# Performance work log

Hardware: AMD Instinct MI355X
Metric: run time of the kernel (lower is better)

## Reference

```python
import jax, jax.numpy as jnp
import numpy as np

B, T, N_EMBD, HEAD = 8, 2048, 1024, 64
NEG_INF = -1e30  # stand-in for float('-inf'), safe under fp16/bf16 after where


def setup_inputs() -> dict:
    key = jax.random.key(0)
    k0, k1, k2, k3 = jax.random.split(key, 4)
    idx = jax.random.normal(k0, (B, T, N_EMBD), dtype=jnp.float32)
    # nn.Linear weights have shape (out_features, in_features)
    Wk = jax.random.normal(k1, (HEAD, N_EMBD), dtype=jnp.float32) * 0.02
    Wq = jax.random.normal(k2, (HEAD, N_EMBD), dtype=jnp.float32) * 0.02
    Wv = jax.random.normal(k3, (HEAD, N_EMBD), dtype=jnp.float32) * 0.02
    return {"idx": idx, "Wk": Wk, "Wq": Wq, "Wv": Wv}


def reference(idx, Wk, Wq, Wv):
    # idx: [B,T,C]; W*: [H,C] (torch Linear layout, y = x @ W.T)
    Tn = idx.shape[1]
    k = jnp.einsum('btc,hc->bth', idx, Wk)
    q = jnp.einsum('btc,hc->bth', idx, Wq)
    v = jnp.einsum('btc,hc->bth', idx, Wv)
    # NOTE: original has NO 1/sqrt(head_size) scaling
    wei = jnp.einsum('bth,bsh->bts', q, k)  # [B,T,T]
    causal = jnp.tril(jnp.ones((Tn, Tn), dtype=bool))  # keep where tril != 0
    wei = jnp.where(causal[None, :, :], wei, NEG_INF)
    # NOTE: original softmaxes over dim=1 (query axis), not the last axis
    wei = jax.nn.softmax(wei, axis=1)
    out = jnp.einsum('bts,bsh->bth', wei, v)  # [B,T,H]
    return out
```

## Files before the change

kernel.cpp:

```cpp
#include <hip/hip_runtime.h>


typedef __attribute__((ext_vector_type(8))) short bf16x8;
typedef __attribute__((ext_vector_type(4))) float f32x4;
typedef unsigned short u16;

#define MFMA(a, b, c) __builtin_amdgcn_mfma_f32_16x16x32_bf16((a), (b), (c), 0, 0, 0)

__device__ __forceinline__ u16 f2bf(float x) {
    unsigned u = __float_as_uint(x);
    u += 0x7fff + ((u >> 16) & 1);
    return (u16)(u >> 16);
}
__device__ __forceinline__ float bf2f(u16 h) {
    return __uint_as_float(((unsigned)h) << 16);
}

__device__ __forceinline__ void split8(const f32x4 x0, const f32x4 x1,
                                       bf16x8* hv, bf16x8* lv)
{
    const float f[8] = {x0[0], x0[1], x0[2], x0[3], x1[0], x1[1], x1[2], x1[3]};
    union { unsigned u[4]; bf16x8 v; } H, L;
    #pragma unroll
    for (int j = 0; j < 4; ++j) {
        const unsigned u0 = __float_as_uint(f[2 * j]);
        const unsigned u1 = __float_as_uint(f[2 * j + 1]);
        H.u[j] = __builtin_amdgcn_perm(u1, u0, 0x07060302);
        const float l0 = f[2 * j]     - __uint_as_float(u0 & 0xffff0000u);
        const float l1 = f[2 * j + 1] - __uint_as_float(u1 & 0xffff0000u);
        L.u[j] = __builtin_amdgcn_perm(__float_as_uint(l1), __float_as_uint(l0),
                                       0x07060302);
    }
    *hv = H.v;
    *lv = L.v;
}

typedef const __attribute__((address_space(1))) void* gas_p;
typedef __attribute__((address_space(3))) void* las_p;

#define WH_OFF  0u
#define WL_OFF  (WH_OFF + 192u*1024u*2u)
#define FQH_OFF (WL_OFF + 192u*1024u*2u)
#define FQL_OFF (FQH_OFF + 2u*1024u*1024u)
#define FKH_OFF (FQL_OFF + 2u*1024u*1024u)
#define FKL_OFF (FKH_OFF + 2u*1024u*1024u)
#define VF_OFF  (FKL_OFF + 2u*1024u*1024u)
#define DD_OFF  (VF_OFF + 2u*1024u*1024u)
#define PF_OFF  (DD_OFF + 8u*2048u*4u)

__global__ __launch_bounds__(128) void wsplit_kernel(
    const float* __restrict__ Wk, const float* __restrict__ Wq,
    const float* __restrict__ Wv, u16* __restrict__ FWH)
{
    const int n = blockIdx.x;
    const int nblk = n >> 4, lr = n & 15;
    const float* src = (n < 64) ? (Wq + (long)n * 1024)
                     : (n < 128) ? (Wk + (long)(n - 64) * 1024)
                                 : (Wv + (long)(n - 128) * 1024);
    const int f = threadIdx.x;
    const int kc = f >> 2, q = f & 3;
    const float4 f0 = *(const float4*)&src[kc * 32 + q * 8];
    const float4 f1 = *(const float4*)&src[kc * 32 + q * 8 + 4];
    const float vs[8] = {f0.x, f0.y, f0.z, f0.w, f1.x, f1.y, f1.z, f1.w};
    bf16x8 hv;
    #pragma unroll
    for (int j = 0; j < 8; ++j) hv[j] = (short)f2bf(vs[j]);
    const long o = ((long)(nblk * 32 + kc) * 64 + q * 16 + lr) * 8;
    *(bf16x8*)&FWH[o] = hv;
}

__global__ __launch_bounds__(512, 2) void qkv_kernel(
    const float* __restrict__ idx, const u16* __restrict__ FWH,
    u16* __restrict__ FQH, u16* __restrict__ FQL,
    u16* __restrict__ FKH, u16* __restrict__ FKL, u16* __restrict__ VF)
{
    __shared__ __align__(16) char smem[3][40960];
    const int tid = threadIdx.x;
    const int w = tid >> 6, lr = tid & 15, quad = (tid >> 4) & 3;
    const int lane = tid & 63;
    const int r0 = blockIdx.x * 64;
    const int b = r0 >> 11, t0 = r0 & 2047;
    const int m0 = (w & 1) * 32;
    const int nbb = (w >> 1) * 3;

    const float* asrc[2];
    int adst[2];
    #pragma unroll
    for (int j = 0; j < 2; ++j) {
        const int s = w * 2 + j;
        const int row = s * 4 + (lane >> 4);
        const int lc = (lane & 15) ^ (row & 7);
        asrc[j] = idx + (long)(r0 + row) * 1024 + lc * 4;
        adst[j] = s * 1024;
    }
    const u16* fsrc[3];
    int fdst[3];
    #pragma unroll
    for (int j = 0; j < 3; ++j) {
        const int seg = w * 3 + j;
        const int nblk = seg >> 1, kcl = seg & 1;
        fsrc[j] = FWH + (long)nblk * 16384 + kcl * 512 + lane * 8;
        fdst[j] = 16384 + seg * 1024;
    }

#define ISSUE(PH)                                                             \
    {                                                                         \
        const int nb_ = (PH) % 3;                                             \
        _Pragma("unroll")                                                     \
        for (int j = 0; j < 2; ++j)                                           \
            __builtin_amdgcn_global_load_lds((gas_p)(asrc[j] + (PH) * 64),    \
                (las_p)(smem[nb_] + adst[j]), 16, 0, 0);                      \
        _Pragma("unroll")                                                     \
        for (int j = 0; j < 3; ++j)                                           \
            __builtin_amdgcn_global_load_lds((gas_p)(fsrc[j] + (long)(PH) * 1024), \
                (las_p)(smem[nb_] + fdst[j]), 16, 0, 0);                      \
    }

#define COMPUTE(PH)                                                           \
    {                                                                         \
        const int nb_ = (PH) % 3;                                             \
        const float* A_ = (const float*)smem[nb_];                            \
        const u16* F_ = (const u16*)(smem[nb_] + 16384);                      \
        _Pragma("unroll")                                                     \
        for (int kc = 0; kc < 2; ++kc) {                                      \
            bf16x8 AH[2], AL[2];                                              \
            _Pragma("unroll")                                                 \
            for (int mi = 0; mi < 2; ++mi) {                                  \
                const int R = m0 + mi * 16 + lr;                              \
                const int c0 = (kc * 8 + quad * 2) ^ (lr & 7);                \
                const f32x4 x0 = *(const f32x4*)&A_[R * 64 + c0 * 4];         \
                const f32x4 x1 = *(const f32x4*)&A_[R * 64 + (c0 ^ 1) * 4];   \
                split8(x0, x1, &AH[mi], &AL[mi]);                             \
            }                                                                 \
            _Pragma("unroll")                                                 \
            for (int nf = 0; nf < 3; ++nf) {                                  \
                const int sb = (((nbb + nf) * 2 + kc)) * 512 + lane * 8;      \
                const bf16x8 bh = *(const bf16x8*)&F_[sb];                    \
                _Pragma("unroll")                                             \
                for (int mi = 0; mi < 2; ++mi) {                              \
                    f32x4 c = acc[mi][nf];                                    \
                    c = MFMA(AH[mi], bh, c);                                  \
                    c = MFMA(AL[mi], bh, c);                                  \
                    acc[mi][nf] = c;                                          \
                }                                                             \
            }                                                                 \
        }                                                                     \
    }

#define WAITV(N)                                                              \
    asm volatile("s_waitcnt vmcnt(" #N ")" ::: "memory");                     \
    __builtin_amdgcn_sched_barrier(0);                                        \
    __builtin_amdgcn_s_barrier();

    f32x4 acc[2][3] = {};

    ISSUE(0); ISSUE(1);
    WAITV(5)

    for (int ph = 0; ph < 14; ++ph) {
        ISSUE(ph + 2);
        __builtin_amdgcn_sched_barrier(0);
        COMPUTE(ph);
        WAITV(5)
    }
    COMPUTE(14);
    WAITV(0)
    COMPUTE(15);

#undef WAITV
#undef COMPUTE
#undef ISSUE

    #pragma unroll
    for (int mi = 0; mi < 2; ++mi) {
        const int tb = t0 + m0 + mi * 16 + quad * 4;
        const int tblk = (t0 + m0 + mi * 16) >> 4;
        #pragma unroll
        for (int nf = 0; nf < 3; ++nf) {
            const int n = (nbb + nf) * 16 + lr;
            const f32x4 a = acc[mi][nf];
            if (n < 128) {
                u16* Hd = (n < 64) ? FQH : FKH;
                u16* Ld = (n < 64) ? FQL : FKL;
                const int h = n & 63;
                const int kc = h >> 5;
                const int lsub = 16 * ((h & 31) >> 3);
                const long base = ((long)(b * 128 + tblk) * 2 + kc) * 512 + (h & 7);
                #pragma unroll
                for (int r = 0; r < 4; ++r) {
                    const float v = a[r];
                    const u16 hi = f2bf(v);
                    const u16 lo = f2bf(v - bf2f(hi));
                    const long o = base + (long)(quad * 4 + r + lsub) * 8;
                    Hd[o] = hi; Ld[o] = lo;
                }
            } else {
                const int h = n - 128;
                const int hblk = h >> 4;
                #pragma unroll
                for (int r = 0; r < 4; ++r) {
                    const int t = tb + r;
                    const long o = ((long)(b * 4 + hblk) * 64 + (t >> 5)) * 512
                                 + (long)(16 * ((t & 31) >> 3) + (h & 15)) * 8 + (t & 7);
                    VF[o] = f2bf(a[r]);
                }
            }
        }
    }
}

__global__ __launch_bounds__(256, 4) void stats_kernel(
    const u16* __restrict__ FQH, const u16* __restrict__ FQL,
    const u16* __restrict__ FKH, const u16* __restrict__ FKL,
    u16* __restrict__ PF, float* __restrict__ D)
{
    __shared__ float red[4][64];
    __shared__ __align__(16) u16 p_l[64 * 64];
    const int tid = threadIdx.x;
    const int w = tid >> 6, lr = tid & 15, quad = (tid >> 4) & 3;
    const int lane = tid & 63;
    const int b = blockIdx.y;
    int x = blockIdx.x, i = 0;
    for (;;) { const int nc = (35 - i) >> 2; if (x < nc) break; x -= nc; ++i; }
    const int s0 = i * 64;
    const int jt0 = i + 4 * x, jt1 = min(jt0 + 4, 32);

    bf16x8 KH[4][2], KL[4][2];
    #pragma unroll
    for (int sf = 0; sf < 4; ++sf) {
        const long kb = ((long)(b * 128 + i * 4 + sf) * 2) * 512 + lane * 8;
        KH[sf][0] = *(const bf16x8*)&FKH[kb];
        KH[sf][1] = *(const bf16x8*)&FKH[kb + 512];
        KL[sf][0] = *(const bf16x8*)&FKL[kb];
        KL[sf][1] = *(const bf16x8*)&FKL[kb + 512];
    }

    float dsum[4][4] = {};
    for (int jt = jt0; jt < jt1; ++jt) {
        const long qb = ((long)(b * 128 + jt * 4 + w) * 2) * 512 + lane * 8;
        const bf16x8 qh0 = *(const bf16x8*)&FQH[qb];
        const bf16x8 qh1 = *(const bf16x8*)&FQH[qb + 512];
        const bf16x8 ql0 = *(const bf16x8*)&FQL[qb];
        const bf16x8 ql1 = *(const bf16x8*)&FQL[qb + 512];
        const bool diag = (jt == i);
        const int t_sub = w * 16 + lr;
        #pragma unroll
        for (int sf = 0; sf < 4; ++sf) {
            f32x4 cc = {};
            cc = MFMA(KH[sf][0], qh0, cc);
            cc = MFMA(KH[sf][0], ql0, cc);
            cc = MFMA(KL[sf][0], qh0, cc);
            cc = MFMA(KH[sf][1], qh1, cc);
            cc = MFMA(KH[sf][1], ql1, cc);
            cc = MFMA(KL[sf][1], qh1, cc);

            u16 hq[4];
            #pragma unroll
            for (int r = 0; r < 4; ++r) {
                float ev = __expf(cc[r]);
                if (diag && (t_sub < sf * 16 + quad * 4 + r)) ev = 0.f;
                dsum[sf][r] += ev;
                hq[r] = f2bf(ev);
            }
            const int s_sub = sf * 16 + quad * 4;
            const int ch = (s_sub >> 3) ^ (t_sub & 7);
            const int aoff = t_sub * 64 + ch * 8 + (s_sub & 7);
            uint2 pk;
            pk.x = (unsigned)hq[0] | ((unsigned)hq[1] << 16);
            pk.y = (unsigned)hq[2] | ((unsigned)hq[3] << 16);
            *(uint2*)&p_l[aoff] = pk;
        }
        __syncthreads();
        #pragma unroll
        for (int kcp = 0; kcp < 2; ++kcp) {
            const int row = w * 16 + (lane & 15);
            const int sc = kcp * 32 + (lane >> 4) * 8;
            const int ch = (sc >> 3) ^ (row & 7);
            const bf16x8 v = *(const bf16x8*)&p_l[row * 64 + ch * 8];
            const long o = ((long)(b * 128 + jt * 4 + w) * 64 + i * 2 + kcp) * 512
                         + lane * 8;
            *(bf16x8*)&PF[o] = v;
        }
        __syncthreads();
    }

    #pragma unroll
    for (int sf = 0; sf < 4; ++sf)
        #pragma unroll
        for (int r = 0; r < 4; ++r) {
            float v = dsum[sf][r];
            v += __shfl_xor(v, 1);
            v += __shfl_xor(v, 2);
            v += __shfl_xor(v, 4);
            v += __shfl_xor(v, 8);
            dsum[sf][r] = v;
        }
    if (lr == 0) {
        #pragma unroll
        for (int sf = 0; sf < 4; ++sf)
            #pragma unroll
            for (int r = 0; r < 4; ++r)
                red[w][sf * 16 + quad * 4 + r] = dsum[sf][r];
    }
    __syncthreads();
    if (tid < 64)
        atomicAdd(&D[b * 2048 + s0 + tid],
                  red[0][tid] + red[1][tid] + red[2][tid] + red[3][tid]);
}

__global__ __launch_bounds__(256) void vscale_kernel(
    u16* __restrict__ VF, const float* __restrict__ D)
{
    const int g = blockIdx.x * 256 + threadIdx.x;
    const long e = (long)g * 8;
    const int lane = (int)((e >> 3) & 63);
    const int kc   = (int)((e >> 9) & 63);
    const int b    = (int)(e >> 17);
    const int s = kc * 32 + (lane >> 4) * 8;
    const float4 d0 = *(const float4*)&D[b * 2048 + s];
    const float4 d1 = *(const float4*)&D[b * 2048 + s + 4];
    const float dv[8] = {d0.x, d0.y, d0.z, d0.w, d1.x, d1.y, d1.z, d1.w};
    bf16x8 vv = *(bf16x8*)&VF[e];
    bf16x8 ov;
    #pragma unroll
    for (int j = 0; j < 8; ++j)
        ov[j] = (short)f2bf(bf2f((u16)vv[j]) / dv[j]);
    *(bf16x8*)&VF[e] = ov;
}

__global__ __launch_bounds__(256, 4) void out_kernel(
    const u16* __restrict__ PF, const u16* __restrict__ VF,
    float* __restrict__ out)
{
    const int tid = threadIdx.x;
    const int w = tid >> 6, lr = tid & 15, quad = (tid >> 4) & 3;
    const int lane = tid & 63;
    const int b = blockIdx.y;
    int x = blockIdx.x, i = 0;
    for (;;) { const int nc = (i + 8) >> 3; if (x < nc) break; x -= nc; ++i; }
    const int t0 = i * 64;
    const int js0 = 8 * x, js1 = min(8 * x + 8, i + 1);
    const int tblk = i * 4 + w;

    f32x4 oacc[4] = {};
    for (int js = js0; js < js1; ++js) {
        const long pb = ((long)(b * 128 + tblk) * 64 + 2 * js) * 512 + lane * 8;
        const bf16x8 a0 = *(const bf16x8*)&PF[pb];
        const bf16x8 a1 = *(const bf16x8*)&PF[pb + 512];
        #pragma unroll
        for (int nf = 0; nf < 4; ++nf) {
            const long vb = ((long)(b * 4 + nf) * 64 + 2 * js) * 512 + lane * 8;
            const bf16x8 v0 = *(const bf16x8*)&VF[vb];
            const bf16x8 v1 = *(const bf16x8*)&VF[vb + 512];
            oacc[nf] = MFMA(a0, v0, oacc[nf]);
            oacc[nf] = MFMA(a1, v1, oacc[nf]);
        }
    }

    const bool single = (i < 8);
    #pragma unroll
    for (int nf = 0; nf < 4; ++nf) {
        const int h = nf * 16 + lr;
        #pragma unroll
        for (int r = 0; r < 4; ++r) {
            const int t = t0 + w * 16 + quad * 4 + r;
            const long o = (long)(b * 2048 + t) * 64 + h;
            if (single) out[o] = oacc[nf][r];
            else        atomicAdd(&out[o], oacc[nf][r]);
        }
    }
}

extern "C" void kernel_launch(void* const* d_in, const int* in_sizes, int n_in,
                              void* d_out, int out_size, void* d_ws, size_t ws_size,
                              hipStream_t stream)
{
    const float* idx = (const float*)d_in[0];
    const float* Wk  = (const float*)d_in[1];
    const float* Wq  = (const float*)d_in[2];
    const float* Wv  = (const float*)d_in[3];
    char* ws = (char*)d_ws;
    float* out = (float*)d_out;

    u16* FWH = (u16*)(ws + WH_OFF);
    u16* FQH = (u16*)(ws + FQH_OFF); u16* FQL = (u16*)(ws + FQL_OFF);
    u16* FKH = (u16*)(ws + FKH_OFF); u16* FKL = (u16*)(ws + FKL_OFF);
    u16* VF  = (u16*)(ws + VF_OFF);
    float* Dp = (float*)(ws + DD_OFF);
    u16* PF  = (u16*)(ws + PF_OFF);

    hipMemsetAsync(out, 0, (size_t)8 * 2048 * 64 * sizeof(float), stream);
    hipMemsetAsync(Dp, 0, (size_t)8 * 2048 * sizeof(float), stream);

    wsplit_kernel<<<192, 128, 0, stream>>>(Wk, Wq, Wv, FWH);
    qkv_kernel<<<256, 512, 0, stream>>>(idx, FWH, FQH, FQL, FKH, FKL, VF);
    stats_kernel<<<dim3(144, 8), 256, 0, stream>>>(FQH, FQL, FKH, FKL, PF, Dp);
    vscale_kernel<<<512, 256, 0, stream>>>(VF, Dp);
    out_kernel<<<dim3(80, 8), 256, 0, stream>>>(PF, VF, out);
}
```

Baseline: 149.8 us.

## Recompute exp(QK) in output kernel instead of storing P matrix

The stats kernel now only accumulates the column softmax denominators and no longer writes the bf16 probability matrix to global memory. The output kernel recomputes the QK^T scores (split-bf16, six MFMAs per tile), exponentiates, masks and stages them through LDS before multiplying with the scaled V. This removes a large global write and read of the T×T probability tiles. In exchange it duplicates the score MFMAs and exp work and adds block barriers and LDS to out_kernel, with its occupancy hint lowered to 2.

```diff
diff --git a/kernel.cpp b/kernel.cpp
--- a/kernel.cpp
+++ b/kernel.cpp
@@ -39,14 +39,12 @@
 typedef __attribute__((address_space(3))) void* las_p;
 
 #define WH_OFF  0u
-#define WL_OFF  (WH_OFF + 192u*1024u*2u)
-#define FQH_OFF (WL_OFF + 192u*1024u*2u)
+#define FQH_OFF (WH_OFF + 2u*192u*1024u*2u)
 #define FQL_OFF (FQH_OFF + 2u*1024u*1024u)
 #define FKH_OFF (FQL_OFF + 2u*1024u*1024u)
 #define FKL_OFF (FKH_OFF + 2u*1024u*1024u)
 #define VF_OFF  (FKL_OFF + 2u*1024u*1024u)
 #define DD_OFF  (VF_OFF + 2u*1024u*1024u)
-#define PF_OFF  (DD_OFF + 8u*2048u*4u)
 
 __global__ __launch_bounds__(128) void wsplit_kernel(
     const float* __restrict__ Wk, const float* __restrict__ Wq,
@@ -212,10 +210,9 @@
 __global__ __launch_bounds__(256, 4) void stats_kernel(
     const u16* __restrict__ FQH, const u16* __restrict__ FQL,
     const u16* __restrict__ FKH, const u16* __restrict__ FKL,
-    u16* __restrict__ PF, float* __restrict__ D)
+    float* __restrict__ D)
 {
     __shared__ float red[4][64];
-    __shared__ __align__(16) u16 p_l[64 * 64];
     const int tid = threadIdx.x;
     const int w = tid >> 6, lr = tid & 15, quad = (tid >> 4) & 3;
     const int lane = tid & 63;
@@ -253,35 +250,13 @@
             cc = MFMA(KH[sf][1], qh1, cc);
             cc = MFMA(KH[sf][1], ql1, cc);
             cc = MFMA(KL[sf][1], qh1, cc);
-
-            u16 hq[4];
             #pragma unroll
             for (int r = 0; r < 4; ++r) {
                 float ev = __expf(cc[r]);
                 if (diag && (t_sub < sf * 16 + quad * 4 + r)) ev = 0.f;
                 dsum[sf][r] += ev;
-                hq[r] = f2bf(ev);
             }
-            const int s_sub = sf * 16 + quad * 4;
-            const int ch = (s_sub >> 3) ^ (t_sub & 7);
-            const int aoff = t_sub * 64 + ch * 8 + (s_sub & 7);
-            uint2 pk;
-            pk.x = (unsigned)hq[0] | ((unsigned)hq[1] << 16);
-            pk.y = (unsigned)hq[2] | ((unsigned)hq[3] << 16);
-            *(uint2*)&p_l[aoff] = pk;
-        }
-        __syncthreads();
-        #pragma unroll
-        for (int kcp = 0; kcp < 2; ++kcp) {
-            const int row = w * 16 + (lane & 15);
-            const int sc = kcp * 32 + (lane >> 4) * 8;
-            const int ch = (sc >> 3) ^ (row & 7);
-            const bf16x8 v = *(const bf16x8*)&p_l[row * 64 + ch * 8];
-            const long o = ((long)(b * 128 + jt * 4 + w) * 64 + i * 2 + kcp) * 512
-                         + lane * 8;
-            *(bf16x8*)&PF[o] = v;
-        }
-        __syncthreads();
+        }
     }
 
     #pragma unroll
@@ -328,10 +303,12 @@
     *(bf16x8*)&VF[e] = ov;
 }
 
-__global__ __launch_bounds__(256, 4) void out_kernel(
-    const u16* __restrict__ PF, const u16* __restrict__ VF,
-    float* __restrict__ out)
-{
+__global__ __launch_bounds__(256, 2) void out_kernel(
+    const u16* __restrict__ FQH, const u16* __restrict__ FQL,
+    const u16* __restrict__ FKH, const u16* __restrict__ FKL,
+    const u16* __restrict__ VF, float* __restrict__ out)
+{
+    __shared__ __align__(16) u16 p_l[64 * 64];
     const int tid = threadIdx.x;
     const int w = tid >> 6, lr = tid & 15, quad = (tid >> 4) & 3;
     const int lane = tid & 63;
@@ -340,21 +317,66 @@
     for (;;) { const int nc = (i + 8) >> 3; if (x < nc) break; x -= nc; ++i; }
     const int t0 = i * 64;
     const int js0 = 8 * x, js1 = min(8 * x + 8, i + 1);
-    const int tblk = i * 4 + w;
+
+    const long qb = ((long)(b * 128 + i * 4 + w) * 2) * 512 + lane * 8;
+    const bf16x8 qh0 = *(const bf16x8*)&FQH[qb];
+    const bf16x8 qh1 = *(const bf16x8*)&FQH[qb + 512];
+    const bf16x8 ql0 = *(const bf16x8*)&FQL[qb];
+    const bf16x8 ql1 = *(const bf16x8*)&FQL[qb + 512];
+    const int t_sub = w * 16 + lr;
 
     f32x4 oacc[4] = {};
     for (int js = js0; js < js1; ++js) {
-        const long pb = ((long)(b * 128 + tblk) * 64 + 2 * js) * 512 + lane * 8;
-        const bf16x8 a0 = *(const bf16x8*)&PF[pb];
-        const bf16x8 a1 = *(const bf16x8*)&PF[pb + 512];
+        const bool diag = (js == i);
+        #pragma unroll
+        for (int sf = 0; sf < 4; ++sf) {
+            const long kb = ((long)(b * 128 + js * 4 + sf) * 2) * 512 + lane * 8;
+            const bf16x8 kh0 = *(const bf16x8*)&FKH[kb];
+            const bf16x8 kh1 = *(const bf16x8*)&FKH[kb + 512];
+            const bf16x8 kl0 = *(const bf16x8*)&FKL[kb];
+            const bf16x8 kl1 = *(const bf16x8*)&FKL[kb + 512];
+            f32x4 cc = {};
+            cc = MFMA(kh0, qh0, cc);
+            cc = MFMA(kh0, ql0, cc);
+            cc = MFMA(kl0, qh0, cc);
+            cc = MFMA(kh1, qh1, cc);
+            cc = MFMA(kh1, ql1, cc);
+            cc = MFMA(kl1, qh1, cc);
+
+            u16 hq[4];
+            #pragma unroll
+            for (int r = 0; r < 4; ++r) {
+                float ev = __expf(cc[r]);
+                if (diag && (t_sub < sf * 16 + quad * 4 + r)) ev = 0.f;
+                hq[r] = f2bf(ev);
+            }
+            const int s_sub = sf * 16 + quad * 4;
+            const int ch = (s_sub >> 3) ^ (t_sub & 7);
+            const int aoff = t_sub * 64 + ch * 8 + (s_sub & 7);
+            uint2 pk;
+            pk.x = (unsigned)hq[0] | ((unsigned)hq[1] << 16);
+            pk.y = (unsigned)hq[2] | ((unsigned)hq[3] << 16);
+            *(uint2*)&p_l[aoff] = pk;
+        }
+        __syncthreads();
+
+        bf16x8 pa[2];
+        #pragma unroll
+        for (int kcp = 0; kcp < 2; ++kcp) {
+            const int row = w * 16 + (lane & 15);
+            const int sc = kcp * 32 + (lane >> 4) * 8;
+            const int ch = (sc >> 3) ^ (row & 7);
+            pa[kcp] = *(const bf16x8*)&p_l[row * 64 + ch * 8];
+        }
         #pragma unroll
         for (int nf = 0; nf < 4; ++nf) {
             const long vb = ((long)(b * 4 + nf) * 64 + 2 * js) * 512 + lane * 8;
             const bf16x8 v0 = *(const bf16x8*)&VF[vb];
             const bf16x8 v1 = *(const bf16x8*)&VF[vb + 512];
-            oacc[nf] = MFMA(a0, v0, oacc[nf]);
-            oacc[nf] = MFMA(a1, v1, oacc[nf]);
-        }
+            oacc[nf] = MFMA(pa[0], v0, oacc[nf]);
+            oacc[nf] = MFMA(pa[1], v1, oacc[nf]);
+        }
+        __syncthreads();
     }
 
     const bool single = (i < 8);
@@ -387,14 +409,13 @@
     u16* FKH = (u16*)(ws + FKH_OFF); u16* FKL = (u16*)(ws + FKL_OFF);
     u16* VF  = (u16*)(ws + VF_OFF);
     float* Dp = (float*)(ws + DD_OFF);
-    u16* PF  = (u16*)(ws + PF_OFF);
 
     hipMemsetAsync(out, 0, (size_t)8 * 2048 * 64 * sizeof(float), stream);
     hipMemsetAsync(Dp, 0, (size_t)8 * 2048 * sizeof(float), stream);
 
     wsplit_kernel<<<192, 128, 0, stream>>>(Wk, Wq, Wv, FWH);
     qkv_kernel<<<256, 512, 0, stream>>>(idx, FWH, FQH, FQL, FKH, FKL, VF);
-    stats_kernel<<<dim3(144, 8), 256, 0, stream>>>(FQH, FQL, FKH, FKL, PF, Dp);
+    stats_kernel<<<dim3(144, 8), 256, 0, stream>>>(FQH, FQL, FKH, FKL, Dp);
     vscale_kernel<<<512, 256, 0, stream>>>(VF, Dp);
-    out_kernel<<<dim3(80, 8), 256, 0, stream>>>(PF, VF, out);
-}
+    out_kernel<<<dim3(80, 8), 256, 0, stream>>>(FQH, FQL, FKH, FKL, VF, out);
+}
```

New measurement: 153.0 us. 2.1% more time.
